# Optimization experiments

Measured on AMD Instinct MI355X. Metric: run time of the kernel, lower is better.

The kernel has to match this reference:

```python
import jax, jax.numpy as jnp
import numpy as np

N = 50000      # nodes
E = 800000     # edges (before self-loops)
F_IN = 128     # input node features
H = 5          # attention heads
C = 32         # per-head channels (hidden_channels // 5)
HC = H * C     # 160 = hidden_channels
G = 64         # graphs in batch


def setup_inputs() -> dict:
    key = jax.random.key(0)
    ks = jax.random.split(key, 20)
    p = lambda k, shape: jax.random.normal(k, shape, dtype=jnp.float32) * 0.1
    return {
        "x": jax.random.normal(ks[0], (N, F_IN), dtype=jnp.float32),
        "edge_index": jax.random.randint(ks[1], (2, E), 0, N),
        "edge_attr": jax.random.normal(ks[2], (E, 1), dtype=jnp.float32),
        "batch": jnp.sort(jax.random.randint(ks[3], (N,), 0, G)),
        # conv1 params (GATConv: lin, lin_edge, att_src, att_dst, att_edge, bias)
        "w1": p(ks[4], (F_IN, HC)), "we1": p(ks[5], (1, HC)),
        "as1": p(ks[6], (H, C)), "ad1": p(ks[7], (H, C)), "ae1": p(ks[8], (H, C)),
        "b1": jnp.zeros((HC,), jnp.float32),
        # conv2 params
        "w2": p(ks[9], (HC, HC)), "we2": p(ks[10], (1, HC)),
        "as2": p(ks[11], (H, C)), "ad2": p(ks[12], (H, C)), "ae2": p(ks[13], (H, C)),
        "b2": jnp.zeros((HC,), jnp.float32),
        # LayerNorms + merge MLP
        "ln1_g": jnp.ones((HC,), jnp.float32), "ln1_b": jnp.zeros((HC,), jnp.float32),
        "ln2_g": jnp.ones((HC,), jnp.float32), "ln2_b": jnp.zeros((HC,), jnp.float32),
        "mw": p(ks[14], (HC, HC)), "mb": jnp.zeros((HC,), jnp.float32),
    }


def _layernorm(x, g, b, eps=1e-5):
    m = x.mean(-1, keepdims=True)
    v = ((x - m) ** 2).mean(-1, keepdims=True)
    return (x - m) / jnp.sqrt(v + eps) * g + b


def _gat_layer(x, edge_index, edge_attr, w, we, a_s, a_d, a_e, b):
    """PyG GATConv with edge_dim, add_self_loops=True, fill_value='mean'."""
    src, dst = edge_index[0], edge_index[1]
    # self-loop edge_attr = mean of incoming edge attrs (scatter-mean onto dst)
    cnt = jax.ops.segment_sum(jnp.ones((E,), x.dtype), dst, num_segments=N)
    ea_mean = jax.ops.segment_sum(edge_attr, dst, num_segments=N) / jnp.maximum(cnt, 1.0)[:, None]
    loop = jnp.arange(N)
    src_f = jnp.concatenate([src, loop])
    dst_f = jnp.concatenate([dst, loop])
    ea_f = jnp.concatenate([edge_attr, ea_mean], axis=0)  # [E+N, 1]

    h = (x @ w).reshape(N, H, C)                           # [N,H,C]
    al_src = jnp.einsum('nhc,hc->nh', h, a_s)              # [N,H]
    al_dst = jnp.einsum('nhc,hc->nh', h, a_d)
    eh = (ea_f @ we).reshape(-1, H, C)                     # [E+N,H,C]
    al_e = jnp.einsum('ehc,hc->eh', eh, a_e)

    alpha = jax.nn.leaky_relu(al_src[src_f] + al_dst[dst_f] + al_e, 0.2)  # [E+N,H]
    amax = jax.ops.segment_max(alpha, dst_f, num_segments=N)
    ex = jnp.exp(alpha - amax[dst_f])
    den = jax.ops.segment_sum(ex, dst_f, num_segments=N)
    alpha = ex / den[dst_f]                                # segment softmax over dst

    out = jax.ops.segment_sum(h[src_f] * alpha[..., None], dst_f, num_segments=N)
    return out.reshape(N, HC) + b, alpha


def reference(x, edge_index, edge_attr, batch,
              w1, we1, as1, ad1, ae1, b1,
              w2, we2, as2, ad2, ae2, b2,
              ln1_g, ln1_b, ln2_g, ln2_b, mw, mb):
    x1, a1 = _gat_layer(x, edge_index, edge_attr, w1, we1, as1, ad1, ae1, b1)
    x1 = jax.nn.leaky_relu(x1, 0.01)
    x1 = _layernorm(x1, ln1_g, ln1_b)          # dropout = identity in eval
    x2, a2 = _gat_layer(x1, edge_index, edge_attr, w2, we2, as2, ad2, ae2, b2)
    x2 = jax.nn.leaky_relu(x2, 0.01)
    x2 = _layernorm(x2, ln2_g, ln2_b)
    x3 = jax.nn.leaky_relu(x2 @ mw + mb, 0.01)
    gcnt = jax.ops.segment_sum(jnp.ones((N,), x3.dtype), batch, num_segments=G)
    pooled = jax.ops.segment_sum(x3, batch, num_segments=G) / jnp.maximum(gcnt, 1.0)[:, None]
    return x3, pooled, a1, a2
```

## Files before the change

### kernel.cpp

```cpp
#include <hip/hip_runtime.h>
#include <hip/hip_fp16.h>
#include <math.h>

#define NN 50000
#define EE 800000
#define FIN 128
#define NH 5
#define HC 160
#define NG 64
#define CH 128
#define NB 160
#define EPB 5000
#define NW 12500
#define ALS8 8
#define LOG2E 1.4426950408889634f

typedef _Float16 f16x8 __attribute__((ext_vector_type(8)));
typedef _Float16 f16x4 __attribute__((ext_vector_type(4)));
typedef float f32x4 __attribute__((ext_vector_type(4)));

__device__ __forceinline__ float lrelu(float x, float s) { return x >= 0.f ? x : s * x; }

__device__ __forceinline__ float4 h8_to_f4(uint2 u) {
    __half2 a = *reinterpret_cast<__half2*>(&u.x);
    __half2 b = *reinterpret_cast<__half2*>(&u.y);
    float2 fa = __half22float2(a), fb = __half22float2(b);
    return make_float4(fa.x, fa.y, fb.x, fb.y);
}

__global__ void prep_kernel(const int* __restrict__ batch, float* psum, int* gcnt,
                            const float* we1, const float* ae1,
                            const float* we2, const float* ae2, float* s_out) {
    int i = blockIdx.x * 256 + threadIdx.x;
    if (i < NG * HC) psum[i] = 0.f;
    if (i < NG) {
        int lo = 0, hi = NN;
        while (lo < hi) { int m = (lo + hi) >> 1; if (batch[m] < i) lo = m + 1; else hi = m; }
        int s = lo;
        lo = 0; hi = NN;
        int g1 = i + 1;
        while (lo < hi) { int m = (lo + hi) >> 1; if (batch[m] < g1) lo = m + 1; else hi = m; }
        gcnt[i] = lo - s;
    }
    if (i < 10) {
        const float* we = (i < 5) ? we1 : we2;
        const float* ae = (i < 5) ? ae1 : ae2;
        int h = i % 5;
        float s = 0.f;
        for (int c = 0; c < 32; c++) s += we[h * 32 + c] * ae[h * 32 + c];
        s_out[i] = s * LOG2E;
    }
}

__global__ void prepw_kernel(const float* __restrict__ w1, const float* __restrict__ w2,
                             const float* __restrict__ mw,
                             __half* wt1, __half* wt2, __half* wt3) {
    int i = blockIdx.x * 256 + threadIdx.x;
    if (i < 160 * 128) {
        int c = i >> 7, k = i & 127;
        wt1[i] = __float2half(w1[k * HC + c]);
    }
    if (i < 160 * 160) {
        int c = i / 160, k = i - c * 160;
        wt2[i] = __float2half(w2[k * HC + c]);
        wt3[i] = __float2half(mw[k * HC + c]);
    }
}

__global__ __launch_bounds__(256) void hist_kernel(const int* __restrict__ ei,
                                                   unsigned* __restrict__ hist_g) {
    __shared__ unsigned lh[NW];
    int b = blockIdx.x, tid = threadIdx.x;
    for (int w = tid; w < NW; w += 256) lh[w] = 0;
    __syncthreads();
    const int* dstp = ei + EE + b * EPB;
    for (int i = tid; i < EPB; i += 256) {
        int d = dstp[i];
        atomicAdd(&lh[d >> 2], 1u << ((d & 3) * 8));
    }
    __syncthreads();
    unsigned* outp = hist_g + (size_t)b * NW;
    for (int w = tid; w < NW; w += 256) outp[w] = lh[w];
}

__global__ void sscan_kernel(const unsigned* __restrict__ hist_g,
                             unsigned short* __restrict__ base_g, int* __restrict__ deg) {
    int w = blockIdx.x * 256 + threadIdx.x;
    if (w >= NW) return;
    unsigned r0 = 0, r1 = 0, r2 = 0, r3 = 0;
    for (int b = 0; b < NB; b++) {
        unsigned x = hist_g[(size_t)b * NW + w];
        uint2 st;
        st.x = r0 | (r1 << 16);
        st.y = r2 | (r3 << 16);
        *reinterpret_cast<uint2*>(&base_g[(size_t)b * NN + 4 * w]) = st;
        r0 += x & 0xffu; r1 += (x >> 8) & 0xffu; r2 += (x >> 16) & 0xffu; r3 += (x >> 24) & 0xffu;
    }
    uint4 dv; dv.x = r0; dv.y = r1; dv.z = r2; dv.w = r3;
    *reinterpret_cast<uint4*>(&deg[4 * w]) = dv;
}

__global__ void scan1_kernel(const int* __restrict__ deg, int* bsum) {
    __shared__ int ws[4];
    int tid = threadIdx.x, lane = tid & 63, wid = tid >> 6;
    int i = blockIdx.x * 256 + tid;
    int v = (i < NN) ? deg[i] : 0;
    for (int o = 32; o >= 1; o >>= 1) v += __shfl_down(v, o, 64);
    if (lane == 0) ws[wid] = v;
    __syncthreads();
    if (tid == 0) bsum[blockIdx.x] = ws[0] + ws[1] + ws[2] + ws[3];
}

__global__ void scan2_kernel(int* bsum, int* boff) {
    __shared__ int ws[4];
    int tid = threadIdx.x, lane = tid & 63, wid = tid >> 6;
    int v = (tid < 196) ? bsum[tid] : 0;
    int x = v;
    for (int o = 1; o < 64; o <<= 1) {
        int t = __shfl_up(x, o, 64);
        if (lane >= o) x += t;
    }
    if (lane == 63) ws[wid] = x;
    __syncthreads();
    if (tid == 0) {
        int acc = 0;
        for (int w = 0; w < 4; w++) { int t = ws[w]; ws[w] = acc; acc += t; }
    }
    __syncthreads();
    if (tid < 196) boff[tid] = x + ws[wid] - v;
}

__global__ void scan3_kernel(const int* __restrict__ deg, const int* __restrict__ boff,
                             int* off) {
    __shared__ int ws[4];
    int tid = threadIdx.x, lane = tid & 63, wid = tid >> 6;
    int i = blockIdx.x * 256 + tid;
    int v = (i < NN) ? deg[i] : 0;
    int x = v;
    for (int o = 1; o < 64; o <<= 1) {
        int t = __shfl_up(x, o, 64);
        if (lane >= o) x += t;
    }
    if (lane == 63) ws[wid] = x;
    __syncthreads();
    if (tid == 0) {
        int acc = 0;
        for (int w = 0; w < 4; w++) { int t = ws[w]; ws[w] = acc; acc += t; }
    }
    __syncthreads();
    int incl = x + ws[wid] + boff[blockIdx.x];
    if (i < NN) off[i + 1] = incl;
    if (i == 0) off[0] = 0;
}

__global__ __launch_bounds__(256) void scatter_kernel(const int* __restrict__ ei,
                                                      const float* __restrict__ ea,
                                                      const unsigned short* __restrict__ base_g,
                                                      const int* __restrict__ soff,
                                                      uint4* __restrict__ erec) {
    __shared__ unsigned lc[NW];
    int b = blockIdx.x, tid = threadIdx.x;
    for (int w = tid; w < NW; w += 256) lc[w] = 0;
    __syncthreads();
    int e0 = b * EPB;
    const unsigned short* brow = base_g + (size_t)b * NN;
    for (int i = tid; i < EPB; i += 256) {
        int e = e0 + i;
        int d = ei[EE + e];
        int sh = (d & 3) * 8;
        unsigned old = atomicAdd(&lc[d >> 2], 1u << sh);
        int r = (int)((old >> sh) & 0xffu);
        int pos = soff[d] + (int)brow[d] + r;
        uint4 rec;
        rec.x = (unsigned)ei[e];
        rec.y = (unsigned)e;
        rec.z = __float_as_uint(ea[e]);
        rec.w = 0;
        erec[pos] = rec;
    }
}

template <int K, typename AT>
__global__ __launch_bounds__(128, 3) void gemm_kernel(const AT* __restrict__ A,
                                                      const __half* __restrict__ Wt,
                                                      const float* __restrict__ a_s,
                                                      const float* __restrict__ a_d,
                                                      __half* __restrict__ out,
                                                      float* __restrict__ al_s,
                                                      float* __restrict__ al_d) {
    __shared__ __align__(16) _Float16 Alds[32 * 40];
    __shared__ __align__(16) _Float16 Bt[160 * 40];
    __shared__ __align__(16) _Float16 Clds[2 * 32 * 88];
    __shared__ float asld[160], adld[160];
    const int tid = threadIdx.x;
    const int w = tid >> 6, l = tid & 63;
    const int lr = l & 15, lq = l >> 4;
    const int base = blockIdx.x * 32;

    for (int i = tid; i < 160; i += 128) { asld[i] = a_s[i]; adld[i] = a_d[i]; }

    f32x4 acc[2][5];
#pragma unroll
    for (int mt = 0; mt < 2; mt++)
#pragma unroll
        for (int t = 0; t < 5; t++) acc[mt][t] = (f32x4){0.f, 0.f, 0.f, 0.f};

    for (int k0 = 0; k0 < K; k0 += 32) {
        __syncthreads();
        if constexpr (sizeof(AT) == 4) {
            for (int f = tid; f < 256; f += 128) {
                int row = f >> 3, q = f & 7;
                float4 av = make_float4(0.f, 0.f, 0.f, 0.f);
                if (base + row < NN)
                    av = *reinterpret_cast<const float4*>(&A[(size_t)(base + row) * K + k0 + q * 4]);
                f16x4 hv = {(_Float16)av.x, (_Float16)av.y, (_Float16)av.z, (_Float16)av.w};
                *reinterpret_cast<f16x4*>(&Alds[row * 40 + q * 4]) = hv;
            }
        } else {
            int row = tid >> 2, q = tid & 3;
            uint4 v = make_uint4(0, 0, 0, 0);
            if (base + row < NN)
                v = *reinterpret_cast<const uint4*>(&A[(size_t)(base + row) * K + k0 + q * 8]);
            *reinterpret_cast<uint4*>(&Alds[row * 40 + q * 8]) = v;
        }
        for (int f = tid; f < 640; f += 128) {
            int c = f >> 2, q = f & 3;
            uint4 v = *reinterpret_cast<const uint4*>(&Wt[(size_t)c * K + k0 + q * 8]);
            *reinterpret_cast<uint4*>(&Bt[c * 40 + q * 8]) = v;
        }
        __syncthreads();
        const f16x8 a0 = *reinterpret_cast<const f16x8*>(&Alds[lr * 40 + lq * 8]);
        const f16x8 a1 = *reinterpret_cast<const f16x8*>(&Alds[(16 + lr) * 40 + lq * 8]);
#pragma unroll
        for (int t = 0; t < 5; t++) {
            const f16x8 b = *reinterpret_cast<const f16x8*>(
                &Bt[((w * 5 + t) * 16 + lr) * 40 + lq * 8]);
            acc[0][t] = __builtin_amdgcn_mfma_f32_16x16x32_f16(a0, b, acc[0][t], 0, 0, 0);
            acc[1][t] = __builtin_amdgcn_mfma_f32_16x16x32_f16(a1, b, acc[1][t], 0, 0, 0);
        }
    }
    _Float16* Cw = Clds + w * (32 * 88);
#pragma unroll
    for (int mt = 0; mt < 2; mt++)
#pragma unroll
        for (int t = 0; t < 5; t++)
#pragma unroll
            for (int j = 0; j < 4; j++)
                Cw[(mt * 16 + lq * 4 + j) * 88 + t * 16 + lr] = (_Float16)acc[mt][t][j];
    __syncthreads();
    for (int i = l; i < 320; i += 64) {
        int row = i / 10, q = i - row * 10;
        if (base + row < NN) {
            uint4 v = *reinterpret_cast<const uint4*>(&Cw[row * 88 + q * 8]);
            *reinterpret_cast<uint4*>(&out[(size_t)(base + row) * HC + w * 80 + q * 8]) = v;
        }
    }
    for (int f = tid; f < 320; f += 128) {
        int row = f / 10, rem = f - row * 10;
        int h = rem >> 1, sd = rem & 1;
        if (base + row < NN) {
            const float* av = (sd ? adld : asld) + h * 32;
            float s = 0.f;
#pragma unroll
            for (int c = 0; c < 32; c++) {
                int col = h * 32 + c;
                int wv = col >= 80;
                s += (float)Clds[wv * (32 * 88) + row * 88 + (col - 80 * wv)] * av[c];
            }
            s *= LOG2E;
            if (sd) al_d[(size_t)(base + row) * NH + h] = s;
            else    al_s[(size_t)(base + row) * ALS8 + h] = s;
        }
    }
}

__global__ __launch_bounds__(256, 8) void aggregate_kernel(
    const int* __restrict__ soff, const uint4* __restrict__ erec,
    const __half* __restrict__ hfeat, const float* __restrict__ als,
    const float* __restrict__ al_d, const float* __restrict__ s_e,
    const float* __restrict__ bias, const float* __restrict__ g_ln,
    const float* __restrict__ b_ln,
    float* __restrict__ alpha_out, __half* __restrict__ x_out) {
    const int wave = threadIdx.x >> 6;
    const int lane = threadIdx.x & 63;
    const int n = blockIdx.x * 4 + wave;
    __shared__ float w_sh_all[4][CH * NH];
    __shared__ int ioff_all[4][CH];
    float* w_sh = w_sh_all[wave];
    int* ioff_sh = ioff_all[wave];

    const int s0 = soff[n];
    const int deg = soff[n + 1] - s0;
    const int items = deg + 1;

    float adr[NH], ser[NH];
#pragma unroll
    for (int h = 0; h < NH; h++) { adr[h] = al_d[n * NH + h]; ser[h] = s_e[h]; }

    const int c0 = 4 * lane;
    const int hd = lane >> 3;
    float4 acc = make_float4(0.f, 0.f, 0.f, 0.f);

    if (items <= CH) {
        float rw[2][NH];
        float lm[NH];
#pragma unroll
        for (int h = 0; h < NH; h++) lm[h] = -3.0e38f;
        float eas = 0.f;
        int myy[2];
#pragma unroll
        for (int t = 0; t < 2; t++) {
            int i = lane + 64 * t;
            if (i < deg) {
                uint4 rec = erec[s0 + i];
                int src = (int)rec.x;
                float eav = __uint_as_float(rec.z);
                ioff_sh[i] = src * (HC * 2);
                myy[t] = (int)rec.y;
                eas += eav;
                const float* ap = als + (size_t)src * ALS8;
                float4 a4 = *reinterpret_cast<const float4*>(ap);
                float a5 = ap[4];
                float asv[5] = {a4.x, a4.y, a4.z, a4.w, a5};
#pragma unroll
                for (int h = 0; h < NH; h++) {
                    float r = lrelu(asv[h] + adr[h] + eav * ser[h], 0.2f);
                    rw[t][h] = r;
                    lm[h] = fmaxf(lm[h], r);
                }
            }
        }
#pragma unroll
        for (int o = 1; o < 64; o <<= 1) {
#pragma unroll
            for (int h = 0; h < NH; h++) lm[h] = fmaxf(lm[h], __shfl_xor(lm[h], o, 64));
            eas += __shfl_xor(eas, o, 64);
        }
        float emean = eas / fmaxf((float)deg, 1.f);
        float m[NH], rs[NH];
        {
            const float* ap = als + (size_t)n * ALS8;
            float4 a4 = *reinterpret_cast<const float4*>(ap);
            float a5 = ap[4];
            float asv[5] = {a4.x, a4.y, a4.z, a4.w, a5};
#pragma unroll
            for (int h = 0; h < NH; h++) {
                rs[h] = lrelu(asv[h] + adr[h] + emean * ser[h], 0.2f);
                m[h] = fmaxf(lm[h], rs[h]);
            }
        }
        float ls[NH] = {0.f, 0.f, 0.f, 0.f, 0.f};
#pragma unroll
        for (int t = 0; t < 2; t++) {
            int i = lane + 64 * t;
            if (i < deg) {
#pragma unroll
                for (int h = 0; h < NH; h++) {
                    float w = exp2f(rw[t][h] - m[h]);
                    rw[t][h] = w;
                    ls[h] += w;
                }
            } else if (i == deg) {
                ioff_sh[i] = n * (HC * 2);
#pragma unroll
                for (int h = 0; h < NH; h++) {
                    float w = exp2f(rs[h] - m[h]);
                    rw[t][h] = w;
                    ls[h] += w;
                }
            }
        }
#pragma unroll
        for (int o = 1; o < 64; o <<= 1) {
#pragma unroll
            for (int h = 0; h < NH; h++) ls[h] += __shfl_xor(ls[h], o, 64);
        }
        float dinv[NH];
#pragma unroll
        for (int h = 0; h < NH; h++) dinv[h] = 1.f / ls[h];
#pragma unroll
        for (int t = 0; t < 2; t++) {
            int i = lane + 64 * t;
            if (i < items) {
                int opos = (i < deg) ? myy[t] : (EE + n);
#pragma unroll
                for (int h = 0; h < NH; h++) {
                    float w = rw[t][h] * dinv[h];
                    w_sh[i * NH + h] = w;
                    alpha_out[(size_t)opos * NH + h] = w;
                }
            }
        }
        __syncthreads();
        if (lane < 40) {
            const char* hb = (const char*)hfeat + (size_t)(c0 * 2);
            for (int i0 = 0; i0 < items; i0 += 4) {
                float wv[4];
                uint2 hv[4];
#pragma unroll
                for (int j = 0; j < 4; j++) {
                    int i = i0 + j;
                    bool ok = i < items;
                    int ii = ok ? i : 0;
                    wv[j] = ok ? w_sh[ii * NH + hd] : 0.f;
                    hv[j] = *reinterpret_cast<const uint2*>(hb + (size_t)(unsigned)ioff_sh[ii]);
                }
#pragma unroll
                for (int j = 0; j < 4; j++) {
                    __half2 p0 = *reinterpret_cast<__half2*>(&hv[j].x);
                    __half2 p1 = *reinterpret_cast<__half2*>(&hv[j].y);
                    acc.x += wv[j] * __low2float(p0);
                    acc.y += wv[j] * __high2float(p0);
                    acc.z += wv[j] * __low2float(p1);
                    acc.w += wv[j] * __high2float(p1);
                }
            }
        }
    } else {
        float lm[NH];
#pragma unroll
        for (int h = 0; h < NH; h++) lm[h] = -3.0e38f;
        float eas = 0.f;
        for (int i = lane; i < deg; i += 64) {
            uint4 rec = erec[s0 + i];
            int src = (int)rec.x;
            float eav = __uint_as_float(rec.z);
            eas += eav;
            const float* ap = als + (size_t)src * ALS8;
            float4 a4 = *reinterpret_cast<const float4*>(ap);
            float a5 = ap[4];
            float asv[5] = {a4.x, a4.y, a4.z, a4.w, a5};
#pragma unroll
            for (int h = 0; h < NH; h++) {
                float r = lrelu(asv[h] + adr[h] + eav * ser[h], 0.2f);
                lm[h] = fmaxf(lm[h], r);
            }
        }
#pragma unroll
        for (int o = 1; o < 64; o <<= 1) {
#pragma unroll
            for (int h = 0; h < NH; h++) lm[h] = fmaxf(lm[h], __shfl_xor(lm[h], o, 64));
            eas += __shfl_xor(eas, o, 64);
        }
        float emean = eas / fmaxf((float)deg, 1.f);
        float m[NH], rs[NH];
        {
            const float* ap = als + (size_t)n * ALS8;
#pragma unroll
            for (int h = 0; h < NH; h++) {
                rs[h] = lrelu(ap[h] + adr[h] + emean * ser[h], 0.2f);
                m[h] = fmaxf(lm[h], rs[h]);
            }
        }
        float ls[NH] = {0.f, 0.f, 0.f, 0.f, 0.f};
        for (int i = lane; i < items; i += 64) {
            int src; float eav;
            if (i < deg) { uint4 rec = erec[s0 + i]; src = (int)rec.x; eav = __uint_as_float(rec.z); }
            else         { src = n; eav = emean; }
            const float* ap = als + (size_t)src * ALS8;
#pragma unroll
            for (int h = 0; h < NH; h++) {
                float r = lrelu(ap[h] + adr[h] + eav * ser[h], 0.2f);
                ls[h] += exp2f(r - m[h]);
            }
        }
#pragma unroll
        for (int o = 1; o < 64; o <<= 1) {
#pragma unroll
            for (int h = 0; h < NH; h++) ls[h] += __shfl_xor(ls[h], o, 64);
        }
        float dinv[NH];
#pragma unroll
        for (int h = 0; h < NH; h++) dinv[h] = 1.f / ls[h];
        __syncthreads();
        for (int i = lane; i < items; i += 64) {
            int src; float eav; int opos;
            if (i < deg) { uint4 rec = erec[s0 + i]; src = (int)rec.x; eav = __uint_as_float(rec.z); opos = (int)rec.y; }
            else         { src = n; eav = emean; opos = EE + n; }
            const float* ap = als + (size_t)src * ALS8;
#pragma unroll
            for (int h = 0; h < NH; h++) {
                float r = lrelu(ap[h] + adr[h] + eav * ser[h], 0.2f);
                alpha_out[(size_t)opos * NH + h] = exp2f(r - m[h]) * dinv[h];
            }
        }
        if (lane < 40) {
            for (int i = 0; i < items; i++) {
                int src; float eav;
                if (i < deg) { uint4 rec = erec[s0 + i]; src = (int)rec.x; eav = __uint_as_float(rec.z); }
                else         { src = n; eav = emean; }
                float r = lrelu(als[(size_t)src * ALS8 + hd] + adr[hd] + eav * ser[hd], 0.2f);
                float w = exp2f(r - m[hd]) * dinv[hd];
                uint2 hv = *reinterpret_cast<const uint2*>(
                    &hfeat[(size_t)src * HC + c0]);
                float4 hf = h8_to_f4(hv);
                acc.x += w * hf.x; acc.y += w * hf.y;
                acc.z += w * hf.z; acc.w += w * hf.w;
            }
        }
    }

    float4 v = make_float4(0.f, 0.f, 0.f, 0.f);
    float p1 = 0.f, p2 = 0.f;
    if (lane < 40) {
        const float4 b4 = *reinterpret_cast<const float4*>(&bias[c0]);
        v.x = lrelu(acc.x + b4.x, 0.01f);
        v.y = lrelu(acc.y + b4.y, 0.01f);
        v.z = lrelu(acc.z + b4.z, 0.01f);
        v.w = lrelu(acc.w + b4.w, 0.01f);
        p1 = v.x + v.y + v.z + v.w;
        p2 = v.x * v.x + v.y * v.y + v.z * v.z + v.w * v.w;
    }
#pragma unroll
    for (int o = 1; o < 64; o <<= 1) {
        p1 += __shfl_xor(p1, o, 64);
        p2 += __shfl_xor(p2, o, 64);
    }
    float mean = p1 * (1.f / (float)HC);
    float var = p2 * (1.f / (float)HC) - mean * mean;
    float rstd = rsqrtf(var + 1e-5f);
    if (lane < 40) {
        const float4 g4 = *reinterpret_cast<const float4*>(&g_ln[c0]);
        const float4 bb = *reinterpret_cast<const float4*>(&b_ln[c0]);
        float ox = (v.x - mean) * rstd * g4.x + bb.x;
        float oy = (v.y - mean) * rstd * g4.y + bb.y;
        float oz = (v.z - mean) * rstd * g4.z + bb.z;
        float ow = (v.w - mean) * rstd * g4.w + bb.w;
        __half2 h01 = __floats2half2_rn(ox, oy);
        __half2 h23 = __floats2half2_rn(oz, ow);
        uint2 st;
        st.x = *reinterpret_cast<unsigned*>(&h01);
        st.y = *reinterpret_cast<unsigned*>(&h23);
        *reinterpret_cast<uint2*>(&x_out[(size_t)n * HC + c0]) = st;
    }
}

__global__ __launch_bounds__(128, 3) void gemm3_kernel(const __half* __restrict__ A,
                                                       const __half* __restrict__ Wt,
                                                       const float* __restrict__ bias,
                                                       const int* __restrict__ batch,
                                                       float* __restrict__ x3,
                                                       float* __restrict__ psum) {
    __shared__ __align__(16) _Float16 Alds[32 * 40];
    __shared__ __align__(16) _Float16 Bt[160 * 40];
    __shared__ int bt[32];
    const int tid = threadIdx.x;
    const int w = tid >> 6, l = tid & 63;
    const int lr = l & 15, lq = l >> 4;
    const int base = blockIdx.x * 32;

    if (tid < 32) bt[tid] = batch[(base + tid < NN) ? (base + tid) : (NN - 1)];

    f32x4 acc[2][5];
#pragma unroll
    for (int mt = 0; mt < 2; mt++)
#pragma unroll
        for (int t = 0; t < 5; t++) acc[mt][t] = (f32x4){0.f, 0.f, 0.f, 0.f};

    for (int k0 = 0; k0 < HC; k0 += 32) {
        __syncthreads();
        {
            int row = tid >> 2, q = tid & 3;
            uint4 v = make_uint4(0, 0, 0, 0);
            if (base + row < NN)
                v = *reinterpret_cast<const uint4*>(&A[(size_t)(base + row) * HC + k0 + q * 8]);
            *reinterpret_cast<uint4*>(&Alds[row * 40 + q * 8]) = v;
        }
        for (int f = tid; f < 640; f += 128) {
            int c = f >> 2, q = f & 3;
            uint4 v = *reinterpret_cast<const uint4*>(&Wt[(size_t)c * HC + k0 + q * 8]);
            *reinterpret_cast<uint4*>(&Bt[c * 40 + q * 8]) = v;
        }
        __syncthreads();
        const f16x8 a0 = *reinterpret_cast<const f16x8*>(&Alds[lr * 40 + lq * 8]);
        const f16x8 a1 = *reinterpret_cast<const f16x8*>(&Alds[(16 + lr) * 40 + lq * 8]);
#pragma unroll
        for (int t = 0; t < 5; t++) {
            const f16x8 b = *reinterpret_cast<const f16x8*>(
                &Bt[((w * 5 + t) * 16 + lr) * 40 + lq * 8]);
            acc[0][t] = __builtin_amdgcn_mfma_f32_16x16x32_f16(a0, b, acc[0][t], 0, 0, 0);
            acc[1][t] = __builtin_amdgcn_mfma_f32_16x16x32_f16(a1, b, acc[1][t], 0, 0, 0);
        }
    }
#pragma unroll
    for (int t = 0; t < 5; t++) {
        int col = w * 80 + t * 16 + lr;
        float bj = bias[col];
        float run = 0.f;
        int g = bt[lq * 4];
#pragma unroll
        for (int mt = 0; mt < 2; mt++)
#pragma unroll
            for (int j = 0; j < 4; j++) {
                int row = mt * 16 + lq * 4 + j;
                bool ok = base + row < NN;
                float vv = lrelu(acc[mt][t][j] + bj, 0.01f);
                if (ok) x3[(size_t)(base + row) * HC + col] = vv;
                int gb = bt[row];
                if (gb != g) { atomicAdd(&psum[g * HC + col], run); run = 0.f; g = gb; }
                if (ok) run += vv;
            }
        atomicAdd(&psum[g * HC + col], run);
    }
}

__global__ void pooldiv_kernel(const float* __restrict__ psum, const int* __restrict__ gcnt,
                               float* pooled_out) {
    int i = blockIdx.x * 256 + threadIdx.x;
    if (i < NG * HC) pooled_out[i] = psum[i] / fmaxf((float)gcnt[i / HC], 1.f);
}

extern "C" void kernel_launch(void* const* d_in, const int* in_sizes, int n_in,
                              void* d_out, int out_size, void* d_ws, size_t ws_size,
                              hipStream_t stream) {
    const float* x    = (const float*)d_in[0];
    const int*   ei   = (const int*)d_in[1];
    const float* ea   = (const float*)d_in[2];
    const int*   batch= (const int*)d_in[3];
    const float* w1   = (const float*)d_in[4];
    const float* we1  = (const float*)d_in[5];
    const float* as1  = (const float*)d_in[6];
    const float* ad1  = (const float*)d_in[7];
    const float* ae1  = (const float*)d_in[8];
    const float* b1   = (const float*)d_in[9];
    const float* w2   = (const float*)d_in[10];
    const float* we2  = (const float*)d_in[11];
    const float* as2  = (const float*)d_in[12];
    const float* ad2  = (const float*)d_in[13];
    const float* ae2  = (const float*)d_in[14];
    const float* b2   = (const float*)d_in[15];
    const float* ln1g = (const float*)d_in[16];
    const float* ln1b = (const float*)d_in[17];
    const float* ln2g = (const float*)d_in[18];
    const float* ln2b = (const float*)d_in[19];
    const float* mw   = (const float*)d_in[20];
    const float* mb   = (const float*)d_in[21];

    float* out = (float*)d_out;
    float* pooled_out = out + (size_t)NN * HC;
    float* a1 = pooled_out + NG * HC;
    float* a2 = a1 + (size_t)(EE + NN) * NH;

    char* wp = (char*)d_ws;
    auto alloc = [&](size_t bytes) {
        void* p = (void*)wp;
        wp += (bytes + 255) & ~(size_t)255;
        return p;
    };
    char* region = (char*)alloc(32 * 1024 * 1024);
    __half* hbuf = (__half*)region;
    __half* x12h = (__half*)(region + 16 * 1024 * 1024);
    unsigned*       hist_g = (unsigned*)region;
    unsigned short* base_g = (unsigned short*)(region + 8 * 1024 * 1024);
    uint4* erec  = (uint4*)alloc((size_t)EE * 16);
    float* als   = (float*)alloc((size_t)NN * ALS8 * 4);
    float* ald   = (float*)alloc((size_t)NN * NH * 4);
    int*   deg   = (int*)alloc((size_t)NN * 4);
    int*   soff  = (int*)alloc((size_t)(NN + 1) * 4);
    float* sbuf  = (float*)alloc(64);
    float* psum  = (float*)alloc((size_t)NG * HC * 4);
    int*   gcnt  = (int*)alloc((size_t)NG * 4);
    int*   bsum  = (int*)alloc(256 * 4);
    int*   boff  = (int*)alloc(256 * 4);
    __half* wt1  = (__half*)alloc((size_t)160 * 128 * 2);
    __half* wt2  = (__half*)alloc((size_t)160 * 160 * 2);
    __half* wt3  = (__half*)alloc((size_t)160 * 160 * 2);

    prep_kernel<<<40, 256, 0, stream>>>(batch, psum, gcnt, we1, ae1, we2, ae2, sbuf);
    prepw_kernel<<<100, 256, 0, stream>>>(w1, w2, mw, wt1, wt2, wt3);
    hist_kernel<<<NB, 256, 0, stream>>>(ei, hist_g);
    sscan_kernel<<<49, 256, 0, stream>>>(hist_g, base_g, deg);
    scan1_kernel<<<196, 256, 0, stream>>>(deg, bsum);
    scan2_kernel<<<1, 256, 0, stream>>>(bsum, boff);
    scan3_kernel<<<196, 256, 0, stream>>>(deg, boff, soff);
    scatter_kernel<<<NB, 256, 0, stream>>>(ei, ea, base_g, soff, erec);

    const int GB = (NN + 31) / 32;

    gemm_kernel<128, float><<<GB, 128, 0, stream>>>(x, wt1, as1, ad1, hbuf, als, ald);
    aggregate_kernel<<<12500, 256, 0, stream>>>(soff, erec, hbuf, als, ald,
                                                sbuf, b1, ln1g, ln1b, a1, x12h);

    gemm_kernel<160, __half><<<GB, 128, 0, stream>>>(x12h, wt2, as2, ad2, hbuf, als, ald);
    aggregate_kernel<<<12500, 256, 0, stream>>>(soff, erec, hbuf, als, ald,
                                                sbuf + 5, b2, ln2g, ln2b, a2, x12h);

    gemm3_kernel<<<GB, 128, 0, stream>>>(x12h, wt3, mb, batch, out, psum);
    pooldiv_kernel<<<40, 256, 0, stream>>>(psum, gcnt, pooled_out);
}
```

Measured before the change: 447.3 us.

## Sort nodes by degree for aggregation and unroll feature gather by eight

Builds a degree histogram and a counting-sort permutation during the CSR scan so that aggregate waves process nodes in descending degree order. This groups similarly sized neighbourhoods within each block to reduce wave imbalance. It also skips the second 64-edge slot when degree is small and raises the gather unroll from 4 to 8 for more loads in flight. The permutation adds atomics in the scan kernels, makes node order within a bin nondeterministic, and scatters output writes.

```diff
diff --git a/kernel.cpp b/kernel.cpp
--- a/kernel.cpp
+++ b/kernel.cpp
@@ -30,9 +30,11 @@
 
 __global__ void prep_kernel(const int* __restrict__ batch, float* psum, int* gcnt,
                             const float* we1, const float* ae1,
-                            const float* we2, const float* ae2, float* s_out) {
+                            const float* we2, const float* ae2, float* s_out,
+                            int* dbin) {
     int i = blockIdx.x * 256 + threadIdx.x;
     if (i < NG * HC) psum[i] = 0.f;
+    if (i < 256) dbin[i] = 0;
     if (i < NG) {
         int lo = 0, hi = NN;
         while (lo < hi) { int m = (lo + hi) >> 1; if (batch[m] < i) lo = m + 1; else hi = m; }
@@ -84,20 +86,32 @@
 }
 
 __global__ void sscan_kernel(const unsigned* __restrict__ hist_g,
-                             unsigned short* __restrict__ base_g, int* __restrict__ deg) {
-    int w = blockIdx.x * 256 + threadIdx.x;
-    if (w >= NW) return;
-    unsigned r0 = 0, r1 = 0, r2 = 0, r3 = 0;
-    for (int b = 0; b < NB; b++) {
-        unsigned x = hist_g[(size_t)b * NW + w];
-        uint2 st;
-        st.x = r0 | (r1 << 16);
-        st.y = r2 | (r3 << 16);
-        *reinterpret_cast<uint2*>(&base_g[(size_t)b * NN + 4 * w]) = st;
-        r0 += x & 0xffu; r1 += (x >> 8) & 0xffu; r2 += (x >> 16) & 0xffu; r3 += (x >> 24) & 0xffu;
-    }
-    uint4 dv; dv.x = r0; dv.y = r1; dv.z = r2; dv.w = r3;
-    *reinterpret_cast<uint4*>(&deg[4 * w]) = dv;
+                             unsigned short* __restrict__ base_g, int* __restrict__ deg,
+                             int* __restrict__ dbin) {
+    __shared__ int lbin[256];
+    int tid = threadIdx.x;
+    int w = blockIdx.x * 256 + tid;
+    lbin[tid] = 0;
+    __syncthreads();
+    if (w < NW) {
+        unsigned r0 = 0, r1 = 0, r2 = 0, r3 = 0;
+        for (int b = 0; b < NB; b++) {
+            unsigned x = hist_g[(size_t)b * NW + w];
+            uint2 st;
+            st.x = r0 | (r1 << 16);
+            st.y = r2 | (r3 << 16);
+            *reinterpret_cast<uint2*>(&base_g[(size_t)b * NN + 4 * w]) = st;
+            r0 += x & 0xffu; r1 += (x >> 8) & 0xffu; r2 += (x >> 16) & 0xffu; r3 += (x >> 24) & 0xffu;
+        }
+        uint4 dv; dv.x = r0; dv.y = r1; dv.z = r2; dv.w = r3;
+        *reinterpret_cast<uint4*>(&deg[4 * w]) = dv;
+        atomicAdd(&lbin[255 - (int)(r0 > 255u ? 255u : r0)], 1);
+        atomicAdd(&lbin[255 - (int)(r1 > 255u ? 255u : r1)], 1);
+        atomicAdd(&lbin[255 - (int)(r2 > 255u ? 255u : r2)], 1);
+        atomicAdd(&lbin[255 - (int)(r3 > 255u ? 255u : r3)], 1);
+    }
+    __syncthreads();
+    if (lbin[tid]) atomicAdd(&dbin[tid], lbin[tid]);
 }
 
 __global__ void scan1_kernel(const int* __restrict__ deg, int* bsum) {
@@ -111,7 +125,8 @@
     if (tid == 0) bsum[blockIdx.x] = ws[0] + ws[1] + ws[2] + ws[3];
 }
 
-__global__ void scan2_kernel(int* bsum, int* boff) {
+__global__ void scan2_kernel(int* bsum, int* boff, const int* __restrict__ dbin,
+                             int* __restrict__ dpos) {
     __shared__ int ws[4];
     int tid = threadIdx.x, lane = tid & 63, wid = tid >> 6;
     int v = (tid < 196) ? bsum[tid] : 0;
@@ -128,10 +143,25 @@
     }
     __syncthreads();
     if (tid < 196) boff[tid] = x + ws[wid] - v;
+    __syncthreads();
+    int bv = dbin[tid];
+    int bx = bv;
+    for (int o = 1; o < 64; o <<= 1) {
+        int t = __shfl_up(bx, o, 64);
+        if (lane >= o) bx += t;
+    }
+    if (lane == 63) ws[wid] = bx;
+    __syncthreads();
+    if (tid == 0) {
+        int acc = 0;
+        for (int w = 0; w < 4; w++) { int t = ws[w]; ws[w] = acc; acc += t; }
+    }
+    __syncthreads();
+    dpos[tid] = bx + ws[wid] - bv;
 }
 
 __global__ void scan3_kernel(const int* __restrict__ deg, const int* __restrict__ boff,
-                             int* off) {
+                             int* off, int* __restrict__ dpos, int* __restrict__ perm) {
     __shared__ int ws[4];
     int tid = threadIdx.x, lane = tid & 63, wid = tid >> 6;
     int i = blockIdx.x * 256 + tid;
@@ -149,7 +179,12 @@
     }
     __syncthreads();
     int incl = x + ws[wid] + boff[blockIdx.x];
-    if (i < NN) off[i + 1] = incl;
+    if (i < NN) {
+        off[i + 1] = incl;
+        int bin = 255 - (v > 255 ? 255 : v);
+        int pos = atomicAdd(&dpos[bin], 1);
+        perm[pos] = i;
+    }
     if (i == 0) off[0] = 0;
 }
 
@@ -275,6 +310,7 @@
 }
 
 __global__ __launch_bounds__(256, 8) void aggregate_kernel(
+    const int* __restrict__ perm,
     const int* __restrict__ soff, const uint4* __restrict__ erec,
     const __half* __restrict__ hfeat, const float* __restrict__ als,
     const float* __restrict__ al_d, const float* __restrict__ s_e,
@@ -283,7 +319,7 @@
     float* __restrict__ alpha_out, __half* __restrict__ x_out) {
     const int wave = threadIdx.x >> 6;
     const int lane = threadIdx.x & 63;
-    const int n = blockIdx.x * 4 + wave;
+    const int n = perm[blockIdx.x * 4 + wave];
     __shared__ float w_sh_all[4][CH * NH];
     __shared__ int ioff_all[4][CH];
     float* w_sh = w_sh_all[wave];
@@ -308,15 +344,14 @@
         for (int h = 0; h < NH; h++) lm[h] = -3.0e38f;
         float eas = 0.f;
         int myy[2];
-#pragma unroll
-        for (int t = 0; t < 2; t++) {
-            int i = lane + 64 * t;
+        {
+            int i = lane;
             if (i < deg) {
                 uint4 rec = erec[s0 + i];
                 int src = (int)rec.x;
                 float eav = __uint_as_float(rec.z);
                 ioff_sh[i] = src * (HC * 2);
-                myy[t] = (int)rec.y;
+                myy[0] = (int)rec.y;
                 eas += eav;
                 const float* ap = als + (size_t)src * ALS8;
                 float4 a4 = *reinterpret_cast<const float4*>(ap);
@@ -325,7 +360,28 @@
 #pragma unroll
                 for (int h = 0; h < NH; h++) {
                     float r = lrelu(asv[h] + adr[h] + eav * ser[h], 0.2f);
-                    rw[t][h] = r;
+                    rw[0][h] = r;
+                    lm[h] = fmaxf(lm[h], r);
+                }
+            }
+        }
+        if (deg > 64) {
+            int i = lane + 64;
+            if (i < deg) {
+                uint4 rec = erec[s0 + i];
+                int src = (int)rec.x;
+                float eav = __uint_as_float(rec.z);
+                ioff_sh[i] = src * (HC * 2);
+                myy[1] = (int)rec.y;
+                eas += eav;
+                const float* ap = als + (size_t)src * ALS8;
+                float4 a4 = *reinterpret_cast<const float4*>(ap);
+                float a5 = ap[4];
+                float asv[5] = {a4.x, a4.y, a4.z, a4.w, a5};
+#pragma unroll
+                for (int h = 0; h < NH; h++) {
+                    float r = lrelu(asv[h] + adr[h] + eav * ser[h], 0.2f);
+                    rw[1][h] = r;
                     lm[h] = fmaxf(lm[h], r);
                 }
             }
@@ -350,14 +406,13 @@
             }
         }
         float ls[NH] = {0.f, 0.f, 0.f, 0.f, 0.f};
-#pragma unroll
-        for (int t = 0; t < 2; t++) {
-            int i = lane + 64 * t;
+        {
+            int i = lane;
             if (i < deg) {
 #pragma unroll
                 for (int h = 0; h < NH; h++) {
-                    float w = exp2f(rw[t][h] - m[h]);
-                    rw[t][h] = w;
+                    float w = exp2f(rw[0][h] - m[h]);
+                    rw[0][h] = w;
                     ls[h] += w;
                 }
             } else if (i == deg) {
@@ -365,11 +420,30 @@
 #pragma unroll
                 for (int h = 0; h < NH; h++) {
                     float w = exp2f(rs[h] - m[h]);
-                    rw[t][h] = w;
+                    rw[0][h] = w;
                     ls[h] += w;
                 }
             }
         }
+        if (deg >= 64) {
+            int i = lane + 64;
+            if (i < deg) {
+#pragma unroll
+                for (int h = 0; h < NH; h++) {
+                    float w = exp2f(rw[1][h] - m[h]);
+                    rw[1][h] = w;
+                    ls[h] += w;
+                }
+            } else if (i == deg) {
+                ioff_sh[i] = n * (HC * 2);
+#pragma unroll
+                for (int h = 0; h < NH; h++) {
+                    float w = exp2f(rs[h] - m[h]);
+                    rw[1][h] = w;
+                    ls[h] += w;
+                }
+            }
+        }
 #pragma unroll
         for (int o = 1; o < 64; o <<= 1) {
 #pragma unroll
@@ -378,14 +452,25 @@
         float dinv[NH];
 #pragma unroll
         for (int h = 0; h < NH; h++) dinv[h] = 1.f / ls[h];
-#pragma unroll
-        for (int t = 0; t < 2; t++) {
-            int i = lane + 64 * t;
+        {
+            int i = lane;
             if (i < items) {
-                int opos = (i < deg) ? myy[t] : (EE + n);
+                int opos = (i < deg) ? myy[0] : (EE + n);
 #pragma unroll
                 for (int h = 0; h < NH; h++) {
-                    float w = rw[t][h] * dinv[h];
+                    float w = rw[0][h] * dinv[h];
+                    w_sh[i * NH + h] = w;
+                    alpha_out[(size_t)opos * NH + h] = w;
+                }
+            }
+        }
+        if (deg >= 64) {
+            int i = lane + 64;
+            if (i < items) {
+                int opos = (i < deg) ? myy[1] : (EE + n);
+#pragma unroll
+                for (int h = 0; h < NH; h++) {
+                    float w = rw[1][h] * dinv[h];
                     w_sh[i * NH + h] = w;
                     alpha_out[(size_t)opos * NH + h] = w;
                 }
@@ -394,11 +479,11 @@
         __syncthreads();
         if (lane < 40) {
             const char* hb = (const char*)hfeat + (size_t)(c0 * 2);
-            for (int i0 = 0; i0 < items; i0 += 4) {
-                float wv[4];
-                uint2 hv[4];
-#pragma unroll
-                for (int j = 0; j < 4; j++) {
+            for (int i0 = 0; i0 < items; i0 += 8) {
+                float wv[8];
+                uint2 hv[8];
+#pragma unroll
+                for (int j = 0; j < 8; j++) {
                     int i = i0 + j;
                     bool ok = i < items;
                     int ii = ok ? i : 0;
@@ -406,7 +491,7 @@
                     hv[j] = *reinterpret_cast<const uint2*>(hb + (size_t)(unsigned)ioff_sh[ii]);
                 }
 #pragma unroll
-                for (int j = 0; j < 4; j++) {
+                for (int j = 0; j < 8; j++) {
                     __half2 p0 = *reinterpret_cast<__half2*>(&hv[j].x);
                     __half2 p1 = *reinterpret_cast<__half2*>(&hv[j].y);
                     acc.x += wv[j] * __low2float(p0);
@@ -662,27 +747,30 @@
     int*   gcnt  = (int*)alloc((size_t)NG * 4);
     int*   bsum  = (int*)alloc(256 * 4);
     int*   boff  = (int*)alloc(256 * 4);
+    int*   dbin  = (int*)alloc(256 * 4);
+    int*   dpos  = (int*)alloc(256 * 4);
+    int*   perm  = (int*)alloc((size_t)NN * 4);
     __half* wt1  = (__half*)alloc((size_t)160 * 128 * 2);
     __half* wt2  = (__half*)alloc((size_t)160 * 160 * 2);
     __half* wt3  = (__half*)alloc((size_t)160 * 160 * 2);
 
-    prep_kernel<<<40, 256, 0, stream>>>(batch, psum, gcnt, we1, ae1, we2, ae2, sbuf);
+    prep_kernel<<<40, 256, 0, stream>>>(batch, psum, gcnt, we1, ae1, we2, ae2, sbuf, dbin);
     prepw_kernel<<<100, 256, 0, stream>>>(w1, w2, mw, wt1, wt2, wt3);
     hist_kernel<<<NB, 256, 0, stream>>>(ei, hist_g);
-    sscan_kernel<<<49, 256, 0, stream>>>(hist_g, base_g, deg);
+    sscan_kernel<<<49, 256, 0, stream>>>(hist_g, base_g, deg, dbin);
     scan1_kernel<<<196, 256, 0, stream>>>(deg, bsum);
-    scan2_kernel<<<1, 256, 0, stream>>>(bsum, boff);
-    scan3_kernel<<<196, 256, 0, stream>>>(deg, boff, soff);
+    scan2_kernel<<<1, 256, 0, stream>>>(bsum, boff, dbin, dpos);
+    scan3_kernel<<<196, 256, 0, stream>>>(deg, boff, soff, dpos, perm);
     scatter_kernel<<<NB, 256, 0, stream>>>(ei, ea, base_g, soff, erec);
 
     const int GB = (NN + 31) / 32;
 
     gemm_kernel<128, float><<<GB, 128, 0, stream>>>(x, wt1, as1, ad1, hbuf, als, ald);
-    aggregate_kernel<<<12500, 256, 0, stream>>>(soff, erec, hbuf, als, ald,
+    aggregate_kernel<<<12500, 256, 0, stream>>>(perm, soff, erec, hbuf, als, ald,
                                                 sbuf, b1, ln1g, ln1b, a1, x12h);
 
     gemm_kernel<160, __half><<<GB, 128, 0, stream>>>(x12h, wt2, as2, ad2, hbuf, als, ald);
-    aggregate_kernel<<<12500, 256, 0, stream>>>(soff, erec, hbuf, als, ald,
+    aggregate_kernel<<<12500, 256, 0, stream>>>(perm, soff, erec, hbuf, als, ald,
                                                 sbuf + 5, b2, ln2g, ln2b, a2, x12h);
 
     gemm3_kernel<<<GB, 128, 0, stream>>>(x12h, wt3, mb, batch, out, psum);
```

New measurement: 572.9 us. 28.1% more time.
